# Kernel tuning notes

Hardware: AMD Instinct MI355X
Metric: run time of the kernel (lower is better)

Reference implementation:

```python
import jax, jax.numpy as jnp
import numpy as np

N, E, L, D = 50000, 800000, 800000, 128
NUM_LAYERS = 3
EPS = 1e-12      # F.normalize eps
SLOPE = 0.01     # leaky_relu default negative slope


def setup_inputs() -> dict:
    key = jax.random.key(0)
    ks = jax.random.split(key, 32)
    s = 0.05
    f32 = jnp.float32
    inp = {
        "node_feature": jax.random.normal(ks[0], (N, D), f32),
        "edge_feature": jax.random.normal(ks[1], (E, D), f32),
        # per-layer stacked weights [num_layers, in, out] (all dims == D)
        "node_Wc": jax.random.normal(ks[2], (NUM_LAYERS, D, D), f32) * s,
        "node_bc": jax.random.normal(ks[3], (NUM_LAYERS, D), f32) * s,
        "node_Wn": jax.random.normal(ks[4], (NUM_LAYERS, D, D), f32) * s,
        "node_bn": jax.random.normal(ks[5], (NUM_LAYERS, D), f32) * s,
        "node_We": jax.random.normal(ks[6], (NUM_LAYERS, D, D), f32) * s,
        "node_be": jax.random.normal(ks[7], (NUM_LAYERS, D), f32) * s,
        "edge_Wc": jax.random.normal(ks[8], (NUM_LAYERS, D, D), f32) * s,
        "edge_bc": jax.random.normal(ks[9], (NUM_LAYERS, D), f32) * s,
        "edge_Wn": jax.random.normal(ks[10], (NUM_LAYERS, D, D), f32) * s,
        "edge_bn": jax.random.normal(ks[11], (NUM_LAYERS, D), f32) * s,
        "edge_We": jax.random.normal(ks[12], (NUM_LAYERS, D, D), f32) * s,
        "edge_be": jax.random.normal(ks[13], (NUM_LAYERS, D), f32) * s,
        # final output linears
        "W_node_out": jax.random.normal(ks[14], (D, D), f32) * s,
        "b_node_out": jax.random.normal(ks[15], (D,), f32) * s,
        "W_edge_out": jax.random.normal(ks[16], (D, D), f32) * s,
        "b_edge_out": jax.random.normal(ks[17], (D,), f32) * s,
        # graph structure (int)
        "edge_index": jax.random.randint(ks[18], (2, E), 0, N),
        "line_edge_index": jax.random.randint(ks[19], (2, L), 0, E),
        "node_edge_index": jax.random.randint(ks[20], (E,), 0, E),
        "node_edge_scatter_index": jax.random.randint(ks[21], (E,), 0, N),
        "edge_node_index": jax.random.randint(ks[22], (L,), 0, N),
        "edge_node_scatter_index": jax.random.randint(ks[23], (L,), 0, E),
    }
    return inp


def _sage(x, ex, ei, ne_idx, ne_scat, Wc, bc, Wn, bn, We, be, num_seg, act):
    # message: gather; aggregate: scatter-sum; update: 3 linears (+bias) fused
    row, col = ei[0], ei[1]
    aggr = jax.ops.segment_sum(x[row], col, num_segments=num_seg)        # [num_seg, D]
    aggr1 = jax.ops.segment_sum(ex[ne_idx], ne_scat, num_segments=num_seg)
    out = (x @ Wc + bc) + (aggr @ Wn + bn) + (aggr1 @ We + be)
    # F.normalize(out, p=2) over last dim with eps clamp
    out = out / jnp.maximum(jnp.linalg.norm(out, axis=-1, keepdims=True), EPS)
    if act:
        out = jnp.where(out >= 0, out, SLOPE * out)  # leaky_relu
    return out


def reference(node_feature, edge_feature,
              node_Wc, node_bc, node_Wn, node_bn, node_We, node_be,
              edge_Wc, edge_bc, edge_Wn, edge_bn, edge_We, edge_be,
              W_node_out, b_node_out, W_edge_out, b_edge_out,
              edge_index, line_edge_index, node_edge_index,
              node_edge_scatter_index, edge_node_index, edge_node_scatter_index):
    nf, ef = node_feature, edge_feature
    for i in range(NUM_LAYERS):
        act = i < NUM_LAYERS - 1  # last layer has activation=None
        temp = nf
        nf = _sage(nf, ef, edge_index, node_edge_index, node_edge_scatter_index,
                   node_Wc[i], node_bc[i], node_Wn[i], node_bn[i], node_We[i], node_be[i],
                   N, act)
        ef = _sage(ef, temp, line_edge_index, edge_node_index, edge_node_scatter_index,
                   edge_Wc[i], edge_bc[i], edge_Wn[i], edge_bn[i], edge_We[i], edge_be[i],
                   E, act)
    tn = nf @ W_node_out + b_node_out   # [N, D]
    te = ef @ W_edge_out + b_edge_out   # [E, D]
    # gmp with a single graph (batch all zeros) == global max pool -> [1, D]
    pooled = jnp.max(tn, axis=0, keepdims=True) + jnp.max(te, axis=0, keepdims=True)
    return (pooled, tn, te)
```

## Files before the change

kernel.cpp:

```cpp
#include <hip/hip_runtime.h>

#define NN 50000
#define EE 800000
#define LL 800000
#define DD 128
#define WSZ (DD * DD)

typedef unsigned short u16;
typedef __attribute__((ext_vector_type(8))) short bf16x8;
typedef __attribute__((ext_vector_type(4))) float f32x4;

__device__ __forceinline__ float bf2f(u16 h) { return __uint_as_float(((unsigned)h) << 16); }
__device__ __forceinline__ u16 f2bf(float x) {
    unsigned u = __float_as_uint(x);
    return (u16)((u + 0x7fffu + ((u >> 16) & 1u)) >> 16);
}

__device__ __forceinline__ unsigned fmap(float x) {
    unsigned u = __float_as_uint(x);
    return (u & 0x80000000u) ? ~u : (u | 0x80000000u);
}
__device__ __forceinline__ float funmap(unsigned u) {
    return (u & 0x80000000u) ? __uint_as_float(u & 0x7fffffffu) : __uint_as_float(~u);
}

__global__ __launch_bounds__(256) void convert_f_kernel(
    const float* __restrict__ in, u16* __restrict__ out, int n4)
{
    int i = blockIdx.x * 256 + threadIdx.x;
    if (i < n4) {
        float4 v = reinterpret_cast<const float4*>(in)[i];
        ushort4 o;
        o.x = f2bf(v.x); o.y = f2bf(v.y); o.z = f2bf(v.z); o.w = f2bf(v.w);
        reinterpret_cast<ushort4*>(out)[i] = o;
    }
}

__global__ __launch_bounds__(256) void convert_w_kernel(
    const float* __restrict__ W, u16* __restrict__ Wt)
{
    const float* w = W + (size_t)blockIdx.x * WSZ;
    u16* o = Wt + (size_t)blockIdx.x * WSZ;
    for (int i = threadIdx.x; i < WSZ; i += 256) {
        int n = i >> 7, k = i & 127;
        o[i] = f2bf(w[k * DD + n]);
    }
}

__global__ __launch_bounds__(256) void hist_kernel(
    const int* __restrict__ dest, int n, int* __restrict__ cnt)
{
    int i = blockIdx.x * 256 + threadIdx.x;
    if (i < n) atomicAdd(&cnt[dest[i]], 1);
}

__global__ __launch_bounds__(256) void scan1_kernel(
    const int* __restrict__ in, int n, int* __restrict__ out, int* __restrict__ bsum)
{
    __shared__ int ts[256];
    const int tid = threadIdx.x;
    const int base = blockIdx.x * 2048 + tid * 8;
    int v[8]; int s = 0;
#pragma unroll
    for (int k = 0; k < 8; ++k) { v[k] = (base + k < n) ? in[base + k] : 0; s += v[k]; }
    ts[tid] = s;
    __syncthreads();
    for (int off = 1; off < 256; off <<= 1) {
        int y = (tid >= off) ? ts[tid - off] : 0;
        __syncthreads();
        ts[tid] += y;
        __syncthreads();
    }
    int excl = ts[tid] - s;
    if (tid == 255) bsum[blockIdx.x] = ts[255];
    int run = excl;
#pragma unroll
    for (int k = 0; k < 8; ++k) { if (base + k < n) out[base + k] = run; run += v[k]; }
}

__global__ __launch_bounds__(512) void scan2_kernel(int* bsum, int nb)
{
    __shared__ int ts[512];
    const int tid = threadIdx.x;
    int v = (tid < nb) ? bsum[tid] : 0;
    ts[tid] = v;
    __syncthreads();
    for (int off = 1; off < 512; off <<= 1) {
        int y = (tid >= off) ? ts[tid - off] : 0;
        __syncthreads();
        ts[tid] += y;
        __syncthreads();
    }
    if (tid < nb) bsum[tid] = ts[tid] - v;
}

__global__ __launch_bounds__(256) void scan3_kernel(
    int* __restrict__ rs, int m, const int* __restrict__ bsum, int total)
{
    int i = blockIdx.x * 256 + threadIdx.x;
    if (i < m) rs[i] += bsum[i >> 11];
    else if (i == m) rs[m] = total;
}

__global__ __launch_bounds__(256) void fill_kernel(
    const int* __restrict__ dest, const int* __restrict__ srcv, int n,
    int* __restrict__ cursor, int* __restrict__ list)
{
    int i = blockIdx.x * 256 + threadIdx.x;
    if (i < n) {
        int p = atomicAdd(&cursor[dest[i]], 1);
        list[p] = srcv[i];
    }
}

__global__ __launch_bounds__(256) void sage_mfma_kernel(
    const u16* __restrict__ x,
    const u16* __restrict__ src0, const int* __restrict__ rs0, const int* __restrict__ ls0,
    const u16* __restrict__ src1, const int* __restrict__ rs1, const int* __restrict__ ls1,
    const u16* __restrict__ Wc, const u16* __restrict__ Wn, const u16* __restrict__ We,
    const float* __restrict__ bc, const float* __restrict__ bn, const float* __restrict__ be,
    u16* __restrict__ out, int M, int act)
{
    __shared__ char smb[32 * 256];
    __shared__ float partial[4][32];
    __shared__ float invs[32];
    const int t = threadIdx.x;
    const int lane = t & 63, g = t >> 6;
    const int l15 = lane & 15, l4 = lane >> 4;
    const int half = lane >> 5, l32 = lane & 31;
    const int block_row = blockIdx.x * 32;
    const int rows_here = min(32, M - block_row);
    const int n0 = g * 32 + l15;

    const f32x4 zero = {0.f, 0.f, 0.f, 0.f};
    f32x4 acc[2][2];
    acc[0][0] = zero; acc[0][1] = zero; acc[1][0] = zero; acc[1][1] = zero;

    {
        const int ar0 = min(block_row + l15, M - 1);
        const int ar1 = min(block_row + 16 + l15, M - 1);
#pragma unroll
        for (int kk = 0; kk < 4; ++kk) {
            int ke = kk * 32 + l4 * 8;
            bf16x8 a0 = *reinterpret_cast<const bf16x8*>(x + (size_t)ar0 * DD + ke);
            bf16x8 a1 = *reinterpret_cast<const bf16x8*>(x + (size_t)ar1 * DD + ke);
            bf16x8 b0 = *reinterpret_cast<const bf16x8*>(Wc + (size_t)n0 * DD + ke);
            bf16x8 b1 = *reinterpret_cast<const bf16x8*>(Wc + (size_t)(n0 + 16) * DD + ke);
            acc[0][0] = __builtin_amdgcn_mfma_f32_16x16x32_bf16(a0, b0, acc[0][0], 0, 0, 0);
            acc[1][0] = __builtin_amdgcn_mfma_f32_16x16x32_bf16(a1, b0, acc[1][0], 0, 0, 0);
            acc[0][1] = __builtin_amdgcn_mfma_f32_16x16x32_bf16(a0, b1, acc[0][1], 0, 0, 0);
            acc[1][1] = __builtin_amdgcn_mfma_f32_16x16x32_bf16(a1, b1, acc[1][1], 0, 0, 0);
        }
    }

    for (int s = 1; s <= 2; ++s) {
        const u16* __restrict__ src = (s == 1) ? src0 : src1;
        const int* __restrict__ rs  = (s == 1) ? rs0  : rs1;
        const int* __restrict__ ls  = (s == 1) ? ls0  : ls1;
        const u16* __restrict__ w   = (s == 1) ? Wn   : We;

        __syncthreads();
        for (int rp = 0; rp < 4; ++rp) {
            int rr = g * 8 + rp * 2 + half;
            float4 a = make_float4(0.f, 0.f, 0.f, 0.f);
            if (rr < rows_here) {
                int d = block_row + rr;
                int beg = rs[d], end = rs[d + 1];
                for (int j = beg; j < end; ++j) {
                    const u16* p = src + (size_t)ls[j] * DD + l32 * 4;
                    ushort4 v = *reinterpret_cast<const ushort4*>(p);
                    a.x += bf2f(v.x); a.y += bf2f(v.y); a.z += bf2f(v.z); a.w += bf2f(v.w);
                }
            }
            ushort4 o;
            o.x = f2bf(a.x); o.y = f2bf(a.y); o.z = f2bf(a.z); o.w = f2bf(a.w);
            int off = (rr * 256 + l32 * 8) ^ ((rr & 7) << 4);
            *reinterpret_cast<ushort4*>(smb + off) = o;
        }
        __syncthreads();

#pragma unroll
        for (int kk = 0; kk < 4; ++kk) {
            int kb = kk * 64 + l4 * 16;
            int off0 = ((l15 * 256) + kb) ^ ((l15 & 7) << 4);
            int off1 = (((16 + l15) * 256) + kb) ^ ((l15 & 7) << 4);
            bf16x8 a0 = *reinterpret_cast<const bf16x8*>(smb + off0);
            bf16x8 a1 = *reinterpret_cast<const bf16x8*>(smb + off1);
            int ke = kk * 32 + l4 * 8;
            bf16x8 b0 = *reinterpret_cast<const bf16x8*>(w + (size_t)n0 * DD + ke);
            bf16x8 b1 = *reinterpret_cast<const bf16x8*>(w + (size_t)(n0 + 16) * DD + ke);
            acc[0][0] = __builtin_amdgcn_mfma_f32_16x16x32_bf16(a0, b0, acc[0][0], 0, 0, 0);
            acc[1][0] = __builtin_amdgcn_mfma_f32_16x16x32_bf16(a1, b0, acc[1][0], 0, 0, 0);
            acc[0][1] = __builtin_amdgcn_mfma_f32_16x16x32_bf16(a0, b1, acc[0][1], 0, 0, 0);
            acc[1][1] = __builtin_amdgcn_mfma_f32_16x16x32_bf16(a1, b1, acc[1][1], 0, 0, 0);
        }
    }

    const int col0 = n0, col1 = n0 + 16;
    const float bs0 = bc[col0] + bn[col0] + be[col0];
    const float bs1 = bc[col1] + bn[col1] + be[col1];
    float vv[2][2][4];
    float ss[8];
#pragma unroll
    for (int a2 = 0; a2 < 2; ++a2)
#pragma unroll
        for (int r = 0; r < 4; ++r) {
            float v0 = acc[a2][0][r] + bs0;
            float v1 = acc[a2][1][r] + bs1;
            vv[a2][0][r] = v0; vv[a2][1][r] = v1;
            ss[a2 * 4 + r] = v0 * v0 + v1 * v1;
        }
#pragma unroll
    for (int m = 1; m <= 8; m <<= 1)
#pragma unroll
        for (int i = 0; i < 8; ++i) ss[i] += __shfl_xor(ss[i], m);
    if (l15 == 0) {
#pragma unroll
        for (int a2 = 0; a2 < 2; ++a2)
#pragma unroll
            for (int r = 0; r < 4; ++r)
                partial[g][a2 * 16 + l4 * 4 + r] = ss[a2 * 4 + r];
    }
    __syncthreads();
    if (t < 32) {
        float s = partial[0][t] + partial[1][t] + partial[2][t] + partial[3][t];
        invs[t] = 1.0f / fmaxf(sqrtf(s), 1e-12f);
    }
    __syncthreads();
#pragma unroll
    for (int a2 = 0; a2 < 2; ++a2)
#pragma unroll
        for (int r = 0; r < 4; ++r) {
            int row = a2 * 16 + l4 * 4 + r;
            float inv = invs[row];
            float v0 = vv[a2][0][r] * inv;
            float v1 = vv[a2][1][r] * inv;
            if (act) {
                v0 = v0 >= 0.f ? v0 : 0.01f * v0;
                v1 = v1 >= 0.f ? v1 : 0.01f * v1;
            }
            if (row < rows_here) {
                size_t ro = (size_t)(block_row + row) * DD;
                out[ro + col0] = f2bf(v0);
                out[ro + col1] = f2bf(v1);
            }
        }
}

__global__ __launch_bounds__(256) void out_mfma_kernel(
    const u16* __restrict__ x, const u16* __restrict__ Wt, const float* __restrict__ bias,
    float* __restrict__ out, unsigned* __restrict__ colmax, int M)
{
    const int t = threadIdx.x;
    const int lane = t & 63, g = t >> 6;
    const int l15 = lane & 15, l4 = lane >> 4;
    const int block_row = blockIdx.x * 32;
    const int rows_here = min(32, M - block_row);
    const int n0 = g * 32 + l15;

    const f32x4 zero = {0.f, 0.f, 0.f, 0.f};
    f32x4 acc[2][2];
    acc[0][0] = zero; acc[0][1] = zero; acc[1][0] = zero; acc[1][1] = zero;

    const int ar0 = min(block_row + l15, M - 1);
    const int ar1 = min(block_row + 16 + l15, M - 1);
#pragma unroll
    for (int kk = 0; kk < 4; ++kk) {
        int ke = kk * 32 + l4 * 8;
        bf16x8 a0 = *reinterpret_cast<const bf16x8*>(x + (size_t)ar0 * DD + ke);
        bf16x8 a1 = *reinterpret_cast<const bf16x8*>(x + (size_t)ar1 * DD + ke);
        bf16x8 b0 = *reinterpret_cast<const bf16x8*>(Wt + (size_t)n0 * DD + ke);
        bf16x8 b1 = *reinterpret_cast<const bf16x8*>(Wt + (size_t)(n0 + 16) * DD + ke);
        acc[0][0] = __builtin_amdgcn_mfma_f32_16x16x32_bf16(a0, b0, acc[0][0], 0, 0, 0);
        acc[1][0] = __builtin_amdgcn_mfma_f32_16x16x32_bf16(a1, b0, acc[1][0], 0, 0, 0);
        acc[0][1] = __builtin_amdgcn_mfma_f32_16x16x32_bf16(a0, b1, acc[0][1], 0, 0, 0);
        acc[1][1] = __builtin_amdgcn_mfma_f32_16x16x32_bf16(a1, b1, acc[1][1], 0, 0, 0);
    }

    const float b0v = bias[n0], b1v = bias[n0 + 16];
    float m0 = -3.402823466e38f, m1 = -3.402823466e38f;
#pragma unroll
    for (int a2 = 0; a2 < 2; ++a2)
#pragma unroll
        for (int r = 0; r < 4; ++r) {
            int row = a2 * 16 + l4 * 4 + r;
            float v0 = acc[a2][0][r] + b0v;
            float v1 = acc[a2][1][r] + b1v;
            if (row < rows_here) {
                size_t ro = (size_t)(block_row + row) * DD;
                out[ro + n0]      = v0;
                out[ro + n0 + 16] = v1;
                m0 = fmaxf(m0, v0);
                m1 = fmaxf(m1, v1);
            }
        }
    m0 = fmaxf(m0, __shfl_xor(m0, 16)); m0 = fmaxf(m0, __shfl_xor(m0, 32));
    m1 = fmaxf(m1, __shfl_xor(m1, 16)); m1 = fmaxf(m1, __shfl_xor(m1, 32));
    if (lane < 16) {
        atomicMax(&colmax[n0], fmap(m0));
        atomicMax(&colmax[n0 + 16], fmap(m1));
    }
}

__global__ void finalize_kernel(const unsigned* __restrict__ colmax, float* __restrict__ pooled)
{
    int j = threadIdx.x;
    if (j < DD) pooled[j] = funmap(colmax[j]) + funmap(colmax[DD + j]);
}

extern "C" void kernel_launch(void* const* d_in, const int* in_sizes, int n_in,
                              void* d_out, int out_size, void* d_ws, size_t ws_size,
                              hipStream_t stream)
{
    const float* nf_in      = (const float*)d_in[0];
    const float* ef_in      = (const float*)d_in[1];
    const float* node_Wc    = (const float*)d_in[2];
    const float* node_bc    = (const float*)d_in[3];
    const float* node_Wn    = (const float*)d_in[4];
    const float* node_bn    = (const float*)d_in[5];
    const float* node_We    = (const float*)d_in[6];
    const float* node_be    = (const float*)d_in[7];
    const float* edge_Wc    = (const float*)d_in[8];
    const float* edge_bc    = (const float*)d_in[9];
    const float* edge_Wn    = (const float*)d_in[10];
    const float* edge_bn    = (const float*)d_in[11];
    const float* edge_We    = (const float*)d_in[12];
    const float* edge_be    = (const float*)d_in[13];
    const float* W_node_out = (const float*)d_in[14];
    const float* b_node_out = (const float*)d_in[15];
    const float* W_edge_out = (const float*)d_in[16];
    const float* b_edge_out = (const float*)d_in[17];
    const int* edge_index        = (const int*)d_in[18];
    const int* line_edge_index   = (const int*)d_in[19];
    const int* node_edge_index   = (const int*)d_in[20];
    const int* node_edge_scatter = (const int*)d_in[21];
    const int* edge_node_index   = (const int*)d_in[22];
    const int* edge_node_scatter = (const int*)d_in[23];

    const size_t ND = (size_t)NN * DD;
    const size_t ED = (size_t)EE * DD;

    u16* nfA = (u16*)d_ws;
    u16* nfB = nfA + ND;
    u16* efA = nfB + ND;
    u16* efB = efA + ED;
    u16* wt  = efB + ED;
    int* ip = (int*)(wt + 20 * WSZ);
    int* cntN0 = ip;  int* rsN0 = cntN0 + NN;  int* curN0 = rsN0 + NN + 1;  int* lstN0 = curN0 + NN;  ip = lstN0 + EE;
    int* cntN1 = ip;  int* rsN1 = cntN1 + NN;  int* curN1 = rsN1 + NN + 1;  int* lstN1 = curN1 + NN;  ip = lstN1 + EE;
    int* cntE0 = ip;  int* rsE0 = cntE0 + EE;  int* curE0 = rsE0 + EE + 1;  int* lstE0 = curE0 + EE;  ip = lstE0 + LL;
    int* cntE1 = ip;  int* rsE1 = cntE1 + EE;  int* curE1 = rsE1 + EE + 1;  int* lstE1 = curE1 + EE;  ip = lstE1 + LL;
    unsigned* colmax = (unsigned*)ip;
    int* bsum = (int*)(colmax + 2 * DD);

    float* tn = (float*)d_out + DD;
    float* te = tn + ND;

    convert_f_kernel<<<(int)((ND / 4 + 255) / 256), 256, 0, stream>>>(nf_in, nfA, (int)(ND / 4));
    convert_f_kernel<<<(int)((ED / 4 + 255) / 256), 256, 0, stream>>>(ef_in, efA, (int)(ED / 4));
    convert_w_kernel<<<3, 256, 0, stream>>>(node_Wc, wt + (size_t)0  * WSZ);
    convert_w_kernel<<<3, 256, 0, stream>>>(node_Wn, wt + (size_t)3  * WSZ);
    convert_w_kernel<<<3, 256, 0, stream>>>(node_We, wt + (size_t)6  * WSZ);
    convert_w_kernel<<<3, 256, 0, stream>>>(edge_Wc, wt + (size_t)9  * WSZ);
    convert_w_kernel<<<3, 256, 0, stream>>>(edge_Wn, wt + (size_t)12 * WSZ);
    convert_w_kernel<<<3, 256, 0, stream>>>(edge_We, wt + (size_t)15 * WSZ);
    convert_w_kernel<<<1, 256, 0, stream>>>(W_node_out, wt + (size_t)18 * WSZ);
    convert_w_kernel<<<1, 256, 0, stream>>>(W_edge_out, wt + (size_t)19 * WSZ);

    auto build = [&](const int* dest, const int* srcv, int n, int m,
                     int* cnt, int* rs, int* cur, int* lst) {
        hipMemsetAsync(cnt, 0, (size_t)m * sizeof(int), stream);
        hist_kernel<<<(n + 255) / 256, 256, 0, stream>>>(dest, n, cnt);
        int nb = (m + 2047) / 2048;
        scan1_kernel<<<nb, 256, 0, stream>>>(cnt, m, rs, bsum);
        scan2_kernel<<<1, 512, 0, stream>>>(bsum, nb);
        scan3_kernel<<<(m + 1 + 255) / 256, 256, 0, stream>>>(rs, m, bsum, n);
        hipMemcpyAsync(cur, rs, (size_t)m * sizeof(int), hipMemcpyDeviceToDevice, stream);
        fill_kernel<<<(n + 255) / 256, 256, 0, stream>>>(dest, srcv, n, cur, lst);
    };
    build(edge_index + EE,      edge_index,      EE, NN, cntN0, rsN0, curN0, lstN0);
    build(node_edge_scatter,    node_edge_index, EE, NN, cntN1, rsN1, curN1, lstN1);
    build(line_edge_index + LL, line_edge_index, LL, EE, cntE0, rsE0, curE0, lstE0);
    build(edge_node_scatter,    edge_node_index, LL, EE, cntE1, rsE1, curE1, lstE1);

    const int gemmN_blocks = (NN + 31) / 32;
    const int gemmE_blocks = (EE + 31) / 32;

    const u16* nf = nfA;
    const u16* ef = efA;
    u16* nfo[3] = { nfB, nfA, nfB };
    u16* efo[3] = { efB, efA, efB };
    for (int i = 0; i < 3; ++i) {
        int act = (i < 2) ? 1 : 0;
        sage_mfma_kernel<<<gemmN_blocks, 256, 0, stream>>>(
            nf, nf, rsN0, lstN0, ef, rsN1, lstN1,
            wt + (size_t)(0 + i) * WSZ, wt + (size_t)(3 + i) * WSZ, wt + (size_t)(6 + i) * WSZ,
            node_bc + (size_t)i * DD, node_bn + (size_t)i * DD, node_be + (size_t)i * DD,
            nfo[i], NN, act);
        sage_mfma_kernel<<<gemmE_blocks, 256, 0, stream>>>(
            ef, ef, rsE0, lstE0, nf, rsE1, lstE1,
            wt + (size_t)(9 + i) * WSZ, wt + (size_t)(12 + i) * WSZ, wt + (size_t)(15 + i) * WSZ,
            edge_bc + (size_t)i * DD, edge_bn + (size_t)i * DD, edge_be + (size_t)i * DD,
            efo[i], EE, act);
        nf = nfo[i];
        ef = efo[i];
    }

    hipMemsetAsync(colmax, 0, 2 * DD * sizeof(unsigned), stream);
    out_mfma_kernel<<<gemmN_blocks, 256, 0, stream>>>(nf, wt + (size_t)18 * WSZ, b_node_out, tn, colmax, NN);
    out_mfma_kernel<<<gemmE_blocks, 256, 0, stream>>>(ef, wt + (size_t)19 * WSZ, b_edge_out, te, colmax + DD, EE);
    finalize_kernel<<<1, DD, 0, stream>>>(colmax, (float*)d_out);
}
```

Baseline: 4.569 ms.

## Fuse final SAGE layer with output linear and stage tile loads/stores through LDS

The last SAGE layer and the output linear plus column-max pooling now run in one kernel. The normalized bf16 tile stays in LDS and is fed straight into a second MFMA pass, so the intermediate layer-3 features are never written to or read back from global memory. The self-feature tile is also loaded cooperatively into LDS with wide loads instead of strided per-lane reads. Output tiles are staged in padded LDS and written as coalesced vector stores. The cost is larger LDS use per block and extra barriers.

```diff
diff --git a/kernel.cpp b/kernel.cpp
--- a/kernel.cpp
+++ b/kernel.cpp
@@ -15,7 +15,6 @@
     unsigned u = __float_as_uint(x);
     return (u16)((u + 0x7fffu + ((u >> 16) & 1u)) >> 16);
 }
-
 __device__ __forceinline__ unsigned fmap(float x) {
     unsigned u = __float_as_uint(x);
     return (u & 0x80000000u) ? ~u : (u | 0x80000000u);
@@ -121,7 +120,7 @@
     const float* __restrict__ bc, const float* __restrict__ bn, const float* __restrict__ be,
     u16* __restrict__ out, int M, int act)
 {
-    __shared__ char smb[32 * 256];
+    __shared__ char smb[8448];
     __shared__ float partial[4][32];
     __shared__ float invs[32];
     const int t = threadIdx.x;
@@ -136,49 +135,42 @@
     f32x4 acc[2][2];
     acc[0][0] = zero; acc[0][1] = zero; acc[1][0] = zero; acc[1][1] = zero;
 
-    {
-        const int ar0 = min(block_row + l15, M - 1);
-        const int ar1 = min(block_row + 16 + l15, M - 1);
-#pragma unroll
-        for (int kk = 0; kk < 4; ++kk) {
-            int ke = kk * 32 + l4 * 8;
-            bf16x8 a0 = *reinterpret_cast<const bf16x8*>(x + (size_t)ar0 * DD + ke);
-            bf16x8 a1 = *reinterpret_cast<const bf16x8*>(x + (size_t)ar1 * DD + ke);
-            bf16x8 b0 = *reinterpret_cast<const bf16x8*>(Wc + (size_t)n0 * DD + ke);
-            bf16x8 b1 = *reinterpret_cast<const bf16x8*>(Wc + (size_t)(n0 + 16) * DD + ke);
-            acc[0][0] = __builtin_amdgcn_mfma_f32_16x16x32_bf16(a0, b0, acc[0][0], 0, 0, 0);
-            acc[1][0] = __builtin_amdgcn_mfma_f32_16x16x32_bf16(a1, b0, acc[1][0], 0, 0, 0);
-            acc[0][1] = __builtin_amdgcn_mfma_f32_16x16x32_bf16(a0, b1, acc[0][1], 0, 0, 0);
-            acc[1][1] = __builtin_amdgcn_mfma_f32_16x16x32_bf16(a1, b1, acc[1][1], 0, 0, 0);
-        }
-    }
-
-    for (int s = 1; s <= 2; ++s) {
-        const u16* __restrict__ src = (s == 1) ? src0 : src1;
-        const int* __restrict__ rs  = (s == 1) ? rs0  : rs1;
-        const int* __restrict__ ls  = (s == 1) ? ls0  : ls1;
-        const u16* __restrict__ w   = (s == 1) ? Wn   : We;
-
+    for (int s = 0; s < 3; ++s) {
+        if (s) __syncthreads();
+        if (s == 0) {
+            const u16* xt = x + (size_t)block_row * DD;
+#pragma unroll
+            for (int p = 0; p < 2; ++p) {
+                int idx = p * 256 + t;
+                int row = idx >> 4, c = idx & 15;
+                uint4 v = *reinterpret_cast<const uint4*>(xt + (size_t)idx * 8);
+                int off = (row * 256 + c * 16) ^ ((row & 7) << 4);
+                *reinterpret_cast<uint4*>(smb + off) = v;
+            }
+        } else {
+            const u16* __restrict__ src = (s == 1) ? src0 : src1;
+            const int* __restrict__ rs  = (s == 1) ? rs0  : rs1;
+            const int* __restrict__ ls  = (s == 1) ? ls0  : ls1;
+            for (int rp = 0; rp < 4; ++rp) {
+                int rr = g * 8 + rp * 2 + half;
+                float4 a = make_float4(0.f, 0.f, 0.f, 0.f);
+                if (rr < rows_here) {
+                    int d = block_row + rr;
+                    int beg = rs[d], end = rs[d + 1];
+                    for (int j = beg; j < end; ++j) {
+                        const u16* p = src + (size_t)ls[j] * DD + l32 * 4;
+                        ushort4 v = *reinterpret_cast<const ushort4*>(p);
+                        a.x += bf2f(v.x); a.y += bf2f(v.y); a.z += bf2f(v.z); a.w += bf2f(v.w);
+                    }
+                }
+                ushort4 o;
+                o.x = f2bf(a.x); o.y = f2bf(a.y); o.z = f2bf(a.z); o.w = f2bf(a.w);
+                int off = (rr * 256 + l32 * 8) ^ ((rr & 7) << 4);
+                *reinterpret_cast<ushort4*>(smb + off) = o;
+            }
+        }
         __syncthreads();
-        for (int rp = 0; rp < 4; ++rp) {
-            int rr = g * 8 + rp * 2 + half;
-            float4 a = make_float4(0.f, 0.f, 0.f, 0.f);
-            if (rr < rows_here) {
-                int d = block_row + rr;
-                int beg = rs[d], end = rs[d + 1];
-                for (int j = beg; j < end; ++j) {
-                    const u16* p = src + (size_t)ls[j] * DD + l32 * 4;
-                    ushort4 v = *reinterpret_cast<const ushort4*>(p);
-                    a.x += bf2f(v.x); a.y += bf2f(v.y); a.z += bf2f(v.z); a.w += bf2f(v.w);
-                }
-            }
-            ushort4 o;
-            o.x = f2bf(a.x); o.y = f2bf(a.y); o.z = f2bf(a.z); o.w = f2bf(a.w);
-            int off = (rr * 256 + l32 * 8) ^ ((rr & 7) << 4);
-            *reinterpret_cast<ushort4*>(smb + off) = o;
-        }
-        __syncthreads();
-
+        const u16* __restrict__ w = (s == 0) ? Wc : ((s == 1) ? Wn : We);
 #pragma unroll
         for (int kk = 0; kk < 4; ++kk) {
             int kb = kk * 64 + l4 * 16;
@@ -196,9 +188,8 @@
         }
     }
 
-    const int col0 = n0, col1 = n0 + 16;
-    const float bs0 = bc[col0] + bn[col0] + be[col0];
-    const float bs1 = bc[col1] + bn[col1] + be[col1];
+    const float bs0 = bc[n0] + bn[n0] + be[n0];
+    const float bs1 = bc[n0 + 16] + bn[n0 + 16] + be[n0 + 16];
     float vv[2][2][4];
     float ss[8];
 #pragma unroll
@@ -227,6 +218,8 @@
         invs[t] = 1.0f / fmaxf(sqrtf(s), 1e-12f);
     }
     __syncthreads();
+
+    u16* ot = (u16*)smb;
 #pragma unroll
     for (int a2 = 0; a2 < 2; ++a2)
 #pragma unroll
@@ -239,21 +232,36 @@
                 v0 = v0 >= 0.f ? v0 : 0.01f * v0;
                 v1 = v1 >= 0.f ? v1 : 0.01f * v1;
             }
-            if (row < rows_here) {
-                size_t ro = (size_t)(block_row + row) * DD;
-                out[ro + col0] = f2bf(v0);
-                out[ro + col1] = f2bf(v1);
-            }
-        }
-}
-
-__global__ __launch_bounds__(256) void out_mfma_kernel(
-    const u16* __restrict__ x, const u16* __restrict__ Wt, const float* __restrict__ bias,
-    float* __restrict__ out, unsigned* __restrict__ colmax, int M)
-{
+            ot[row * 132 + n0]      = f2bf(v0);
+            ot[row * 132 + n0 + 16] = f2bf(v1);
+        }
+    __syncthreads();
+#pragma unroll
+    for (int p = 0; p < 4; ++p) {
+        int idx = p * 256 + t;
+        int row = idx >> 5, c = idx & 31;
+        if (row < rows_here)
+            *reinterpret_cast<ushort4*>(out + (size_t)(block_row + row) * DD + c * 4)
+                = *reinterpret_cast<const ushort4*>(ot + row * 132 + c * 4);
+    }
+}
+
+__global__ __launch_bounds__(256) void sage_out_mfma_kernel(
+    const u16* __restrict__ x,
+    const u16* __restrict__ src0, const int* __restrict__ rs0, const int* __restrict__ ls0,
+    const u16* __restrict__ src1, const int* __restrict__ rs1, const int* __restrict__ ls1,
+    const u16* __restrict__ Wc, const u16* __restrict__ Wn, const u16* __restrict__ We,
+    const float* __restrict__ bc, const float* __restrict__ bn, const float* __restrict__ be,
+    const u16* __restrict__ Wo, const float* __restrict__ bo,
+    float* __restrict__ tout, unsigned* __restrict__ colmax, int M)
+{
+    __shared__ char smb[16896];
+    __shared__ float partial[4][32];
+    __shared__ float invs[32];
     const int t = threadIdx.x;
     const int lane = t & 63, g = t >> 6;
     const int l15 = lane & 15, l4 = lane >> 4;
+    const int half = lane >> 5, l32 = lane & 31;
     const int block_row = blockIdx.x * 32;
     const int rows_here = min(32, M - block_row);
     const int n0 = g * 32 + l15;
@@ -262,43 +270,149 @@
     f32x4 acc[2][2];
     acc[0][0] = zero; acc[0][1] = zero; acc[1][0] = zero; acc[1][1] = zero;
 
-    const int ar0 = min(block_row + l15, M - 1);
-    const int ar1 = min(block_row + 16 + l15, M - 1);
-#pragma unroll
-    for (int kk = 0; kk < 4; ++kk) {
-        int ke = kk * 32 + l4 * 8;
-        bf16x8 a0 = *reinterpret_cast<const bf16x8*>(x + (size_t)ar0 * DD + ke);
-        bf16x8 a1 = *reinterpret_cast<const bf16x8*>(x + (size_t)ar1 * DD + ke);
-        bf16x8 b0 = *reinterpret_cast<const bf16x8*>(Wt + (size_t)n0 * DD + ke);
-        bf16x8 b1 = *reinterpret_cast<const bf16x8*>(Wt + (size_t)(n0 + 16) * DD + ke);
-        acc[0][0] = __builtin_amdgcn_mfma_f32_16x16x32_bf16(a0, b0, acc[0][0], 0, 0, 0);
-        acc[1][0] = __builtin_amdgcn_mfma_f32_16x16x32_bf16(a1, b0, acc[1][0], 0, 0, 0);
-        acc[0][1] = __builtin_amdgcn_mfma_f32_16x16x32_bf16(a0, b1, acc[0][1], 0, 0, 0);
-        acc[1][1] = __builtin_amdgcn_mfma_f32_16x16x32_bf16(a1, b1, acc[1][1], 0, 0, 0);
-    }
-
-    const float b0v = bias[n0], b1v = bias[n0 + 16];
-    float m0 = -3.402823466e38f, m1 = -3.402823466e38f;
+    for (int s = 0; s < 3; ++s) {
+        if (s) __syncthreads();
+        if (s == 0) {
+            const u16* xt = x + (size_t)block_row * DD;
+#pragma unroll
+            for (int p = 0; p < 2; ++p) {
+                int idx = p * 256 + t;
+                int row = idx >> 4, c = idx & 15;
+                uint4 v = *reinterpret_cast<const uint4*>(xt + (size_t)idx * 8);
+                int off = (row * 256 + c * 16) ^ ((row & 7) << 4);
+                *reinterpret_cast<uint4*>(smb + off) = v;
+            }
+        } else {
+            const u16* __restrict__ src = (s == 1) ? src0 : src1;
+            const int* __restrict__ rs  = (s == 1) ? rs0  : rs1;
+            const int* __restrict__ ls  = (s == 1) ? ls0  : ls1;
+            for (int rp = 0; rp < 4; ++rp) {
+                int rr = g * 8 + rp * 2 + half;
+                float4 a = make_float4(0.f, 0.f, 0.f, 0.f);
+                if (rr < rows_here) {
+                    int d = block_row + rr;
+                    int beg = rs[d], end = rs[d + 1];
+                    for (int j = beg; j < end; ++j) {
+                        const u16* p = src + (size_t)ls[j] * DD + l32 * 4;
+                        ushort4 v = *reinterpret_cast<const ushort4*>(p);
+                        a.x += bf2f(v.x); a.y += bf2f(v.y); a.z += bf2f(v.z); a.w += bf2f(v.w);
+                    }
+                }
+                ushort4 o;
+                o.x = f2bf(a.x); o.y = f2bf(a.y); o.z = f2bf(a.z); o.w = f2bf(a.w);
+                int off = (rr * 256 + l32 * 8) ^ ((rr & 7) << 4);
+                *reinterpret_cast<ushort4*>(smb + off) = o;
+            }
+        }
+        __syncthreads();
+        const u16* __restrict__ w = (s == 0) ? Wc : ((s == 1) ? Wn : We);
+#pragma unroll
+        for (int kk = 0; kk < 4; ++kk) {
+            int kb = kk * 64 + l4 * 16;
+            int off0 = ((l15 * 256) + kb) ^ ((l15 & 7) << 4);
+            int off1 = (((16 + l15) * 256) + kb) ^ ((l15 & 7) << 4);
+            bf16x8 a0 = *reinterpret_cast<const bf16x8*>(smb + off0);
+            bf16x8 a1 = *reinterpret_cast<const bf16x8*>(smb + off1);
+            int ke = kk * 32 + l4 * 8;
+            bf16x8 b0 = *reinterpret_cast<const bf16x8*>(w + (size_t)n0 * DD + ke);
+            bf16x8 b1 = *reinterpret_cast<const bf16x8*>(w + (size_t)(n0 + 16) * DD + ke);
+            acc[0][0] = __builtin_amdgcn_mfma_f32_16x16x32_bf16(a0, b0, acc[0][0], 0, 0, 0);
+            acc[1][0] = __builtin_amdgcn_mfma_f32_16x16x32_bf16(a1, b0, acc[1][0], 0, 0, 0);
+            acc[0][1] = __builtin_amdgcn_mfma_f32_16x16x32_bf16(a0, b1, acc[0][1], 0, 0, 0);
+            acc[1][1] = __builtin_amdgcn_mfma_f32_16x16x32_bf16(a1, b1, acc[1][1], 0, 0, 0);
+        }
+    }
+
+    const float bs0 = bc[n0] + bn[n0] + be[n0];
+    const float bs1 = bc[n0 + 16] + bn[n0 + 16] + be[n0 + 16];
+    float vv[2][2][4];
+    float ss[8];
+#pragma unroll
+    for (int a2 = 0; a2 < 2; ++a2)
+#pragma unroll
+        for (int r = 0; r < 4; ++r) {
+            float v0 = acc[a2][0][r] + bs0;
+            float v1 = acc[a2][1][r] + bs1;
+            vv[a2][0][r] = v0; vv[a2][1][r] = v1;
+            ss[a2 * 4 + r] = v0 * v0 + v1 * v1;
+        }
+#pragma unroll
+    for (int m = 1; m <= 8; m <<= 1)
+#pragma unroll
+        for (int i = 0; i < 8; ++i) ss[i] += __shfl_xor(ss[i], m);
+    if (l15 == 0) {
+#pragma unroll
+        for (int a2 = 0; a2 < 2; ++a2)
+#pragma unroll
+            for (int r = 0; r < 4; ++r)
+                partial[g][a2 * 16 + l4 * 4 + r] = ss[a2 * 4 + r];
+    }
+    __syncthreads();
+    if (t < 32) {
+        float s = partial[0][t] + partial[1][t] + partial[2][t] + partial[3][t];
+        invs[t] = 1.0f / fmaxf(sqrtf(s), 1e-12f);
+    }
+    __syncthreads();
 #pragma unroll
     for (int a2 = 0; a2 < 2; ++a2)
 #pragma unroll
         for (int r = 0; r < 4; ++r) {
             int row = a2 * 16 + l4 * 4 + r;
-            float v0 = acc[a2][0][r] + b0v;
-            float v1 = acc[a2][1][r] + b1v;
-            if (row < rows_here) {
-                size_t ro = (size_t)(block_row + row) * DD;
-                out[ro + n0]      = v0;
-                out[ro + n0 + 16] = v1;
-                m0 = fmaxf(m0, v0);
-                m1 = fmaxf(m1, v1);
-            }
+            float inv = invs[row];
+            int o0 = (row * 256 + n0 * 2) ^ ((row & 7) << 4);
+            int o1 = (row * 256 + (n0 + 16) * 2) ^ ((row & 7) << 4);
+            *reinterpret_cast<u16*>(smb + o0) = f2bf(vv[a2][0][r] * inv);
+            *reinterpret_cast<u16*>(smb + o1) = f2bf(vv[a2][1][r] * inv);
+        }
+    __syncthreads();
+
+    f32x4 acc2[2][2];
+    acc2[0][0] = zero; acc2[0][1] = zero; acc2[1][0] = zero; acc2[1][1] = zero;
+#pragma unroll
+    for (int kk = 0; kk < 4; ++kk) {
+        int kb = kk * 64 + l4 * 16;
+        int off0 = ((l15 * 256) + kb) ^ ((l15 & 7) << 4);
+        int off1 = (((16 + l15) * 256) + kb) ^ ((l15 & 7) << 4);
+        bf16x8 a0 = *reinterpret_cast<const bf16x8*>(smb + off0);
+        bf16x8 a1 = *reinterpret_cast<const bf16x8*>(smb + off1);
+        int ke = kk * 32 + l4 * 8;
+        bf16x8 b0 = *reinterpret_cast<const bf16x8*>(Wo + (size_t)n0 * DD + ke);
+        bf16x8 b1 = *reinterpret_cast<const bf16x8*>(Wo + (size_t)(n0 + 16) * DD + ke);
+        acc2[0][0] = __builtin_amdgcn_mfma_f32_16x16x32_bf16(a0, b0, acc2[0][0], 0, 0, 0);
+        acc2[1][0] = __builtin_amdgcn_mfma_f32_16x16x32_bf16(a1, b0, acc2[1][0], 0, 0, 0);
+        acc2[0][1] = __builtin_amdgcn_mfma_f32_16x16x32_bf16(a0, b1, acc2[0][1], 0, 0, 0);
+        acc2[1][1] = __builtin_amdgcn_mfma_f32_16x16x32_bf16(a1, b1, acc2[1][1], 0, 0, 0);
+    }
+
+    const float b0v = bo[n0], b1v = bo[n0 + 16];
+    float m0 = -3.402823466e38f, m1 = -3.402823466e38f;
+    float* ft = (float*)smb;
+    __syncthreads();
+#pragma unroll
+    for (int a2 = 0; a2 < 2; ++a2)
+#pragma unroll
+        for (int r = 0; r < 4; ++r) {
+            int row = a2 * 16 + l4 * 4 + r;
+            float v0 = acc2[a2][0][r] + b0v;
+            float v1 = acc2[a2][1][r] + b1v;
+            ft[row * 132 + n0]      = v0;
+            ft[row * 132 + n0 + 16] = v1;
+            if (row < rows_here) { m0 = fmaxf(m0, v0); m1 = fmaxf(m1, v1); }
         }
     m0 = fmaxf(m0, __shfl_xor(m0, 16)); m0 = fmaxf(m0, __shfl_xor(m0, 32));
     m1 = fmaxf(m1, __shfl_xor(m1, 16)); m1 = fmaxf(m1, __shfl_xor(m1, 32));
     if (lane < 16) {
         atomicMax(&colmax[n0], fmap(m0));
         atomicMax(&colmax[n0 + 16], fmap(m1));
+    }
+    __syncthreads();
+#pragma unroll
+    for (int p = 0; p < 4; ++p) {
+        int idx = p * 256 + t;
+        int row = idx >> 5, c = idx & 31;
+        if (row < rows_here)
+            *reinterpret_cast<float4*>(tout + (size_t)(block_row + row) * DD + c * 4)
+                = *reinterpret_cast<const float4*>(ft + row * 132 + c * 4);
     }
 }
 
@@ -388,26 +502,33 @@
 
     const u16* nf = nfA;
     const u16* ef = efA;
-    u16* nfo[3] = { nfB, nfA, nfB };
-    u16* efo[3] = { efB, efA, efB };
-    for (int i = 0; i < 3; ++i) {
-        int act = (i < 2) ? 1 : 0;
+    u16* nfo[2] = { nfB, nfA };
+    u16* efo[2] = { efB, efA };
+    for (int i = 0; i < 2; ++i) {
         sage_mfma_kernel<<<gemmN_blocks, 256, 0, stream>>>(
             nf, nf, rsN0, lstN0, ef, rsN1, lstN1,
             wt + (size_t)(0 + i) * WSZ, wt + (size_t)(3 + i) * WSZ, wt + (size_t)(6 + i) * WSZ,
             node_bc + (size_t)i * DD, node_bn + (size_t)i * DD, node_be + (size_t)i * DD,
-            nfo[i], NN, act);
+            nfo[i], NN, 1);
         sage_mfma_kernel<<<gemmE_blocks, 256, 0, stream>>>(
             ef, ef, rsE0, lstE0, nf, rsE1, lstE1,
             wt + (size_t)(9 + i) * WSZ, wt + (size_t)(12 + i) * WSZ, wt + (size_t)(15 + i) * WSZ,
             edge_bc + (size_t)i * DD, edge_bn + (size_t)i * DD, edge_be + (size_t)i * DD,
-            efo[i], EE, act);
+            efo[i], EE, 1);
         nf = nfo[i];
         ef = efo[i];
     }
 
     hipMemsetAsync(colmax, 0, 2 * DD * sizeof(unsigned), stream);
-    out_mfma_kernel<<<gemmN_blocks, 256, 0, stream>>>(nf, wt + (size_t)18 * WSZ, b_node_out, tn, colmax, NN);
-    out_mfma_kernel<<<gemmE_blocks, 256, 0, stream>>>(ef, wt + (size_t)19 * WSZ, b_edge_out, te, colmax + DD, EE);
+    sage_out_mfma_kernel<<<gemmN_blocks, 256, 0, stream>>>(
+        nf, nf, rsN0, lstN0, ef, rsN1, lstN1,
+        wt + (size_t)2 * WSZ, wt + (size_t)5 * WSZ, wt + (size_t)8 * WSZ,
+        node_bc + (size_t)2 * DD, node_bn + (size_t)2 * DD, node_be + (size_t)2 * DD,
+        wt + (size_t)18 * WSZ, b_node_out, tn, colmax, NN);
+    sage_out_mfma_kernel<<<gemmE_blocks, 256, 0, stream>>>(
+        ef, ef, rsE0, lstE0, nf, rsE1, lstE1,
+        wt + (size_t)11 * WSZ, wt + (size_t)14 * WSZ, wt + (size_t)17 * WSZ,
+        edge_bc + (size_t)2 * DD, edge_bn + (size_t)2 * DD, edge_be + (size_t)2 * DD,
+        wt + (size_t)19 * WSZ, b_edge_out, te, colmax + DD, EE);
     finalize_kernel<<<1, DD, 0, stream>>>(colmax, (float*)d_out);
 }
```

Measured after the change: 3.903 ms. 1.17x faster.
